# Kernel optimization log

Measured on AMD Instinct MI355X. Metric: run time of the kernel, lower is better.

## Reference

```python
import jax, jax.numpy as jnp
import numpy as np

N_NODES = 50000
N_POOLED = 25000
N_EDGES = 800000
D = 64
NUM_LAYERS = 4
LN_EPS = 1e-5
LEAKY_SLOPE = 0.01


def setup_inputs() -> dict:
    key = jax.random.key(0)
    k_x, k_e, k_i, k_w = jax.random.split(key, 4)
    x = jax.random.normal(k_x, (N_POOLED, D), dtype=jnp.float32)
    edge_index = jax.random.randint(k_e, (2, N_EDGES), 0, N_NODES, dtype=jnp.int64)
    # unique sorted indices of kept nodes (as produced by top-k pooling)
    perm = jax.random.permutation(k_i, N_NODES)
    idx = jnp.sort(perm[:N_POOLED]).astype(jnp.int64)
    Ws = jax.random.normal(k_w, (NUM_LAYERS, D, D), dtype=jnp.float32) / np.sqrt(D)
    bs = jnp.zeros((NUM_LAYERS, D), dtype=jnp.float32)
    gammas = jnp.ones((NUM_LAYERS, D), dtype=jnp.float32)
    betas = jnp.zeros((NUM_LAYERS, D), dtype=jnp.float32)
    return {"x": x, "edge_index": edge_index, "idx": idx,
            "Ws": Ws, "bs": bs, "gammas": gammas, "betas": betas}


def _layer_norm(x, gamma, beta):
    mu = jnp.mean(x, axis=-1, keepdims=True)
    xc = x - mu
    var = jnp.mean(xc * xc, axis=-1, keepdims=True)
    return xc * jax.lax.rsqrt(var + LN_EPS) * gamma + beta


def reference(x, edge_index, idx, Ws, bs, gammas, betas):
    # Unpool (layer 0): scatter pooled features into full-size zero tensor.
    cur = jnp.zeros((N_NODES, D), dtype=x.dtype).at[idx].set(x)

    # GCN normalization with self loops (shared across layers; graph is fixed).
    loop = jnp.arange(N_NODES, dtype=edge_index.dtype)
    src = jnp.concatenate([edge_index[0], loop])
    dst = jnp.concatenate([edge_index[1], loop])
    deg = jax.ops.segment_sum(jnp.ones_like(dst, dtype=x.dtype), dst,
                              num_segments=N_NODES)
    dinv = jax.lax.rsqrt(jnp.maximum(deg, 1.0))  # deg >= 1 (self loops)
    norm = (dinv[src] * dinv[dst])[:, None]      # [E+N, 1]

    h = None
    for l in range(NUM_LAYERS):
        # GCNConv: X W, then D^{-1/2}(A+I)D^{-1/2} aggregation, then bias.
        xw = cur @ Ws[l]
        agg = jax.ops.segment_sum(xw[src] * norm, dst, num_segments=N_NODES)
        agg = agg + bs[l]
        y = _layer_norm(agg, gammas[l], betas[l])
        act = jnp.where(y > 0, y, LEAKY_SLOPE * y)  # LeakyReLU(0.01)
        # dropout p=0.3 is identity in eval mode
        h = act * 0.5 if h is None else h + act * 0.5
        cur = act  # subsequent unpools are identity (sizes already match)
    return h
```

## Files before the change

kernel.cpp:

```cpp
#include <hip/hip_runtime.h>
#include <hip/hip_fp16.h>

#define NN 50000
#define NP 25000
#define NE 800000
#define DD 64
#define NL 4


__device__ __forceinline__ ushort f2bf(float f) {
    unsigned u = __float_as_uint(f);
    unsigned r = (u + 0x7fffu + ((u >> 16) & 1u)) >> 16;
    return (ushort)r;
}

__device__ __forceinline__ float4 bf4_to_f4(uint a, uint b) {
    float4 r;
    r.x = __uint_as_float(a << 16);
    r.y = __uint_as_float(a & 0xffff0000u);
    r.z = __uint_as_float(b << 16);
    r.w = __uint_as_float(b & 0xffff0000u);
    return r;
}

__device__ __forceinline__ float4 ld_bf16x4(const uint2* p) {
    uint2 q = *p;
    return bf4_to_f4(q.x, q.y);
}


__global__ void count_edges_k(const int* __restrict__ dst, int* __restrict__ cnt,
                              int* __restrict__ rank, int E) {
    int e = blockIdx.x * 256 + threadIdx.x;
    if (e < E) rank[e] = atomicAdd(&cnt[dst[e]], 1);
}

__global__ void scan_local_k(const int* __restrict__ cnt, int* __restrict__ rowptr,
                             int* __restrict__ bsum, int n) {
    __shared__ int tmp[1024];
    int t = threadIdx.x;
    int i = blockIdx.x * 1024 + t;
    int v = (i < n) ? cnt[i] : 0;
    tmp[t] = v;
    __syncthreads();
    for (int off = 1; off < 1024; off <<= 1) {
        int a = (t >= off) ? tmp[t - off] : 0;
        __syncthreads();
        tmp[t] += a;
        __syncthreads();
    }
    if (i < n) rowptr[i] = tmp[t] - v;
    if (t == 1023) bsum[blockIdx.x] = tmp[1023];
}

__global__ void finalize_k(int* __restrict__ rowptr, const int* __restrict__ bsum,
                           const int* __restrict__ cnt, float* __restrict__ dinv,
                           int n, int nb) {
    __shared__ int base_sh, total_sh;
    int t = threadIdx.x;
    if (t < 64) {
        int v = (t < nb) ? bsum[t] : 0;
        int s = v;
#pragma unroll
        for (int o = 1; o < 64; o <<= 1) {
            int u = __shfl_up(s, o);
            if (t >= o) s += u;
        }
        if (t == (int)blockIdx.x) base_sh = s - v;
        if (t == nb - 1) total_sh = s;
    }
    __syncthreads();
    int i = blockIdx.x * 1024 + t;
    if (i < n) {
        rowptr[i] += base_sh;
        dinv[i] = rsqrtf((float)(cnt[i] + 1));
    }
    if (i == n) rowptr[n] = total_sh;
}

__global__ void fill_scatter_k(const int* __restrict__ src, const int* __restrict__ dst,
                               const int* __restrict__ rank, const int* __restrict__ rowptr,
                               const float* __restrict__ dinv, uint* __restrict__ csr,
                               const float4* __restrict__ x4, const int* __restrict__ idx,
                               ushort4* __restrict__ c0) {
    int b = blockIdx.x;
    if (b < 3125) {
        int e = b * 256 + threadIdx.x;
        int s = src[e], d = dst[e];
        int p = rowptr[d] + rank[e];
        float w = dinv[s] * dinv[d];
        uint h = (uint)__half_as_ushort(__float2half_rn(w));
        csr[p] = (uint)s | (h << 16);
    } else {
        int i = (b - 3125) * 256 + threadIdx.x;
        if (i >= NP * 16) return;
        int row = i >> 4, q = i & 15;
        float4 v = x4[i];
        ushort4 o;
        o.x = f2bf(v.x); o.y = f2bf(v.y); o.z = f2bf(v.z); o.w = f2bf(v.w);
        c0[(size_t)idx[row] * 16 + q] = o;
    }
}


__global__ void gemm64_k(const uint2* __restrict__ in2, const float* __restrict__ W,
                         ushort* __restrict__ out) {
    __shared__ float sW[64][64];
    __shared__ float srow[16][64];
    int t = threadIdx.x;
    const float4* W4 = (const float4*)W;
    float4* sW4 = (float4*)sW;
#pragma unroll
    for (int j = 0; j < 4; ++j) sW4[t + 256 * j] = W4[t + 256 * j];
    int r0 = blockIdx.x * 16;
    float4 val = ld_bf16x4(in2 + (size_t)r0 * 16 + t);
    *(float4*)&srow[t >> 4][4 * (t & 15)] = val;
    __syncthreads();
    int r = t >> 4;
    int c4 = (t & 15) * 4;
    float ax = 0.f, ay = 0.f, az = 0.f, aw = 0.f;
#pragma unroll
    for (int k = 0; k < 64; ++k) {
        float a = srow[r][k];
        float4 w = *(const float4*)&sW[k][c4];
        ax += a * w.x; ay += a * w.y; az += a * w.z; aw += a * w.w;
    }
    ushort4 o;
    o.x = f2bf(ax); o.y = f2bf(ay); o.z = f2bf(az); o.w = f2bf(aw);
    *(ushort4*)&out[(size_t)(r0 + r) * 64 + c4] = o;
}


__global__ void agg_ln_k(const uint4* __restrict__ xw4, const int* __restrict__ rowptr,
                         const uint* __restrict__ csr, const float* __restrict__ dinv,
                         const float4* __restrict__ bias4, const float4* __restrict__ gamma4,
                         const float4* __restrict__ beta4, uint4* next,
                         const uint4* c1, const uint4* c2, const uint4* c3,
                         float4* outp, int last) {
    int tid = threadIdx.x;
    int l8 = tid & 7;
    int v = blockIdx.x * 32 + (tid >> 3);
    if (v >= NN) return;
    float dv = dinv[v];
    int jb = rowptr[v], je = rowptr[v + 1];
    float4 aLo, aHi;
    {
        uint4 q = xw4[(size_t)v * 8 + l8];
        float4 lo = bf4_to_f4(q.x, q.y), hi = bf4_to_f4(q.z, q.w);
        float s = dv * dv;
        aLo.x = s * lo.x; aLo.y = s * lo.y; aLo.z = s * lo.z; aLo.w = s * lo.w;
        aHi.x = s * hi.x; aHi.y = s * hi.y; aHi.z = s * hi.z; aHi.w = s * hi.w;
    }
#define WGT(E)  __half2float(__ushort_as_half((ushort)((E) >> 16)))
    for (int j = jb; j < je; j += 8) {
        uint e0 = csr[j];
        uint e1 = csr[min(j + 1, je - 1)];
        uint e2 = csr[min(j + 2, je - 1)];
        uint e3 = csr[min(j + 3, je - 1)];
        uint e4 = csr[min(j + 4, je - 1)];
        uint e5 = csr[min(j + 5, je - 1)];
        uint e6 = csr[min(j + 6, je - 1)];
        uint e7 = csr[min(j + 7, je - 1)];
        float w0 = WGT(e0);
        float w1 = (j + 1 < je) ? WGT(e1) : 0.f;
        float w2 = (j + 2 < je) ? WGT(e2) : 0.f;
        float w3 = (j + 3 < je) ? WGT(e3) : 0.f;
        float w4 = (j + 4 < je) ? WGT(e4) : 0.f;
        float w5 = (j + 5 < je) ? WGT(e5) : 0.f;
        float w6 = (j + 6 < je) ? WGT(e6) : 0.f;
        float w7 = (j + 7 < je) ? WGT(e7) : 0.f;
        uint4 q0 = xw4[(size_t)(e0 & 0xffffu) * 8 + l8];
        uint4 q1 = xw4[(size_t)(e1 & 0xffffu) * 8 + l8];
        uint4 q2 = xw4[(size_t)(e2 & 0xffffu) * 8 + l8];
        uint4 q3 = xw4[(size_t)(e3 & 0xffffu) * 8 + l8];
        uint4 q4 = xw4[(size_t)(e4 & 0xffffu) * 8 + l8];
        uint4 q5 = xw4[(size_t)(e5 & 0xffffu) * 8 + l8];
        uint4 q6 = xw4[(size_t)(e6 & 0xffffu) * 8 + l8];
        uint4 q7 = xw4[(size_t)(e7 & 0xffffu) * 8 + l8];
#define ACC(Q, W) { \
        float4 lo = bf4_to_f4(Q.x, Q.y), hi = bf4_to_f4(Q.z, Q.w); \
        aLo.x += W * lo.x; aLo.y += W * lo.y; aLo.z += W * lo.z; aLo.w += W * lo.w; \
        aHi.x += W * hi.x; aHi.y += W * hi.y; aHi.z += W * hi.z; aHi.w += W * hi.w; }
        ACC(q0, w0) ACC(q1, w1) ACC(q2, w2) ACC(q3, w3)
        ACC(q4, w4) ACC(q5, w5) ACC(q6, w6) ACC(q7, w7)
#undef ACC
    }
#undef WGT
    float4 bLo = bias4[2 * l8], bBhi = bias4[2 * l8 + 1];
    aLo.x += bLo.x; aLo.y += bLo.y; aLo.z += bLo.z; aLo.w += bLo.w;
    aHi.x += bBhi.x; aHi.y += bBhi.y; aHi.z += bBhi.z; aHi.w += bBhi.w;
    float s = aLo.x + aLo.y + aLo.z + aLo.w + aHi.x + aHi.y + aHi.z + aHi.w;
#pragma unroll
    for (int o = 1; o <= 4; o <<= 1) s += __shfl_xor(s, o);
    float mu = s * (1.0f / 64.0f);
    float4 cLo = make_float4(aLo.x - mu, aLo.y - mu, aLo.z - mu, aLo.w - mu);
    float4 cHi = make_float4(aHi.x - mu, aHi.y - mu, aHi.z - mu, aHi.w - mu);
    float q2v = cLo.x * cLo.x + cLo.y * cLo.y + cLo.z * cLo.z + cLo.w * cLo.w
              + cHi.x * cHi.x + cHi.y * cHi.y + cHi.z * cHi.z + cHi.w * cHi.w;
#pragma unroll
    for (int o = 1; o <= 4; o <<= 1) q2v += __shfl_xor(q2v, o);
    float rs = rsqrtf(q2v * (1.0f / 64.0f) + 1e-5f);
    float4 gLo = gamma4[2 * l8], gHi = gamma4[2 * l8 + 1];
    float4 tLo = beta4[2 * l8],  tHi = beta4[2 * l8 + 1];
    float4 yLo = make_float4(cLo.x * rs * gLo.x + tLo.x, cLo.y * rs * gLo.y + tLo.y,
                             cLo.z * rs * gLo.z + tLo.z, cLo.w * rs * gLo.w + tLo.w);
    float4 yHi = make_float4(cHi.x * rs * gHi.x + tHi.x, cHi.y * rs * gHi.y + tHi.y,
                             cHi.z * rs * gHi.z + tHi.z, cHi.w * rs * gHi.w + tHi.w);
    float4 eLo = make_float4(yLo.x > 0.f ? yLo.x : 0.01f * yLo.x,
                             yLo.y > 0.f ? yLo.y : 0.01f * yLo.y,
                             yLo.z > 0.f ? yLo.z : 0.01f * yLo.z,
                             yLo.w > 0.f ? yLo.w : 0.01f * yLo.w);
    float4 eHi = make_float4(yHi.x > 0.f ? yHi.x : 0.01f * yHi.x,
                             yHi.y > 0.f ? yHi.y : 0.01f * yHi.y,
                             yHi.z > 0.f ? yHi.z : 0.01f * yHi.z,
                             yHi.w > 0.f ? yHi.w : 0.01f * yHi.w);
    if (!last) {
        uint4 o;
        o.x = (uint)f2bf(eLo.x) | ((uint)f2bf(eLo.y) << 16);
        o.y = (uint)f2bf(eLo.z) | ((uint)f2bf(eLo.w) << 16);
        o.z = (uint)f2bf(eHi.x) | ((uint)f2bf(eHi.y) << 16);
        o.w = (uint)f2bf(eHi.z) | ((uint)f2bf(eHi.w) << 16);
        next[(size_t)v * 8 + l8] = o;
    } else {
        uint4 u1 = c1[(size_t)v * 8 + l8];
        uint4 u2 = c2[(size_t)v * 8 + l8];
        uint4 u3 = c3[(size_t)v * 8 + l8];
        float4 p1 = bf4_to_f4(u1.x, u1.y), p1h = bf4_to_f4(u1.z, u1.w);
        float4 p2 = bf4_to_f4(u2.x, u2.y), p2h = bf4_to_f4(u2.z, u2.w);
        float4 p3 = bf4_to_f4(u3.x, u3.y), p3h = bf4_to_f4(u3.z, u3.w);
        float4 oLo, oHi;
        oLo.x = 0.5f * (p1.x + p2.x + p3.x + eLo.x);
        oLo.y = 0.5f * (p1.y + p2.y + p3.y + eLo.y);
        oLo.z = 0.5f * (p1.z + p2.z + p3.z + eLo.z);
        oLo.w = 0.5f * (p1.w + p2.w + p3.w + eLo.w);
        oHi.x = 0.5f * (p1h.x + p2h.x + p3h.x + eHi.x);
        oHi.y = 0.5f * (p1h.y + p2h.y + p3h.y + eHi.y);
        oHi.z = 0.5f * (p1h.z + p2h.z + p3h.z + eHi.z);
        oHi.w = 0.5f * (p1h.w + p2h.w + p3h.w + eHi.w);
        outp[(size_t)v * 16 + 2 * l8]     = oLo;
        outp[(size_t)v * 16 + 2 * l8 + 1] = oHi;
    }
}


extern "C" void kernel_launch(void* const* d_in, const int* in_sizes, int n_in,
                              void* d_out, int out_size, void* d_ws, size_t ws_size,
                              hipStream_t stream) {
    const float* x      = (const float*)d_in[0];
    const int*   ei     = (const int*)d_in[1];
    const int*   src    = ei;
    const int*   dst    = ei + NE;
    const int*   idx    = (const int*)d_in[2];
    const float* Ws     = (const float*)d_in[3];
    const float* bs     = (const float*)d_in[4];
    const float* gammas = (const float*)d_in[5];
    const float* betas  = (const float*)d_in[6];
    float* out = (float*)d_out;

    char* w = (char*)d_ws;
    auto alloc = [&](size_t bytes) -> char* {
        char* p = w;
        w += (bytes + 255) & ~(size_t)255;
        return p;
    };
    char*   zbase  = w;
    int*    cnt    = (int*)alloc((size_t)NN * 4);
    ushort* c0     = (ushort*)alloc((size_t)NN * 64 * 2);
    size_t  zbytes = (size_t)(w - zbase);
    ushort* c[NL];
    c[0] = c0;
    for (int l = 1; l < NL; ++l) c[l] = (ushort*)alloc((size_t)NN * 64 * 2);
    ushort* xw     = (ushort*)alloc((size_t)NN * 64 * 2);
    int*    rowptr = (int*)alloc((size_t)(NN + 1) * 4);
    int*    rank   = (int*)alloc((size_t)NE * 4);
    float*  dinv   = (float*)alloc((size_t)NN * 4);
    int*    bsum   = (int*)alloc(64 * 4);
    uint*   csr    = (uint*)alloc((size_t)NE * 4);

    hipMemsetAsync(zbase, 0, zbytes, stream);

    count_edges_k<<<(NE + 255) / 256, 256, 0, stream>>>(dst, cnt, rank, NE);
    int nb = (NN + 1023) / 1024;
    scan_local_k<<<nb, 1024, 0, stream>>>(cnt, rowptr, bsum, NN);
    finalize_k<<<nb, 1024, 0, stream>>>(rowptr, bsum, cnt, dinv, NN, nb);
    fill_scatter_k<<<3125 + 1563, 256, 0, stream>>>(src, dst, rank, rowptr, dinv, csr,
                                                    (const float4*)x, idx, (ushort4*)c[0]);

    int agrid = (NN + 31) / 32;
    for (int l = 0; l < NL; ++l) {
        gemm64_k<<<NN / 16, 256, 0, stream>>>((const uint2*)c[l], Ws + (size_t)l * 64 * 64,
                                              xw);
        int last = (l == NL - 1);
        agg_ln_k<<<agrid, 256, 0, stream>>>((const uint4*)xw, rowptr, csr, dinv,
                                            (const float4*)(bs + l * 64),
                                            (const float4*)(gammas + l * 64),
                                            (const float4*)(betas + l * 64),
                                            last ? nullptr : (uint4*)c[l + 1],
                                            (const uint4*)c[1], (const uint4*)c[2],
                                            (const uint4*)c[3], (float4*)out, last);
    }
}
```

Before: 200.0 us.

## Fuse GEMM into aggregation kernel by aggregating before multiplying by W

```diff
diff --git a/kernel.cpp b/kernel.cpp
--- a/kernel.cpp
+++ b/kernel.cpp
@@ -21,11 +21,6 @@
     r.z = __uint_as_float(b << 16);
     r.w = __uint_as_float(b & 0xffff0000u);
     return r;
-}
-
-__device__ __forceinline__ float4 ld_bf16x4(const uint2* p) {
-    uint2 q = *p;
-    return bf4_to_f4(q.x, q.y);
 }
 
 
@@ -103,98 +98,98 @@
 }
 
 
-__global__ void gemm64_k(const uint2* __restrict__ in2, const float* __restrict__ W,
-                         ushort* __restrict__ out) {
+__global__ void agg_mm_ln_k(const uint4* __restrict__ cur4, const int* __restrict__ rowptr,
+                            const uint* __restrict__ csr, const float* __restrict__ dinv,
+                            const float* __restrict__ W,
+                            const float4* __restrict__ bias4,
+                            const float4* __restrict__ gamma4,
+                            const float4* __restrict__ beta4, uint4* next,
+                            const uint4* c1, const uint4* c2, const uint4* c3,
+                            float4* outp, int last) {
     __shared__ float sW[64][64];
-    __shared__ float srow[16][64];
+    __shared__ float sz[32][68];
     int t = threadIdx.x;
-    const float4* W4 = (const float4*)W;
-    float4* sW4 = (float4*)sW;
-#pragma unroll
-    for (int j = 0; j < 4; ++j) sW4[t + 256 * j] = W4[t + 256 * j];
-    int r0 = blockIdx.x * 16;
-    float4 val = ld_bf16x4(in2 + (size_t)r0 * 16 + t);
-    *(float4*)&srow[t >> 4][4 * (t & 15)] = val;
+    {
+        const float4* W4 = (const float4*)W;
+        float4* sW4 = (float4*)sW;
+#pragma unroll
+        for (int j = 0; j < 4; ++j) sW4[t + 256 * j] = W4[t + 256 * j];
+    }
+    int l8 = t & 7;
+    int oct = t >> 3;
+    int v = blockIdx.x * 32 + oct;
+    float4 aLo = make_float4(0.f, 0.f, 0.f, 0.f);
+    float4 aHi = make_float4(0.f, 0.f, 0.f, 0.f);
+    if (v < NN) {
+        float dv = dinv[v];
+        int jb = rowptr[v], je = rowptr[v + 1];
+        {
+            uint4 q = cur4[(size_t)v * 8 + l8];
+            float4 lo = bf4_to_f4(q.x, q.y), hi = bf4_to_f4(q.z, q.w);
+            float s = dv * dv;
+            aLo.x = s * lo.x; aLo.y = s * lo.y; aLo.z = s * lo.z; aLo.w = s * lo.w;
+            aHi.x = s * hi.x; aHi.y = s * hi.y; aHi.z = s * hi.z; aHi.w = s * hi.w;
+        }
+#define WGT(E)  __half2float(__ushort_as_half((ushort)((E) >> 16)))
+        for (int j = jb; j < je; j += 8) {
+            uint e0 = csr[j];
+            uint e1 = csr[min(j + 1, je - 1)];
+            uint e2 = csr[min(j + 2, je - 1)];
+            uint e3 = csr[min(j + 3, je - 1)];
+            uint e4 = csr[min(j + 4, je - 1)];
+            uint e5 = csr[min(j + 5, je - 1)];
+            uint e6 = csr[min(j + 6, je - 1)];
+            uint e7 = csr[min(j + 7, je - 1)];
+            float w0 = WGT(e0);
+            float w1 = (j + 1 < je) ? WGT(e1) : 0.f;
+            float w2 = (j + 2 < je) ? WGT(e2) : 0.f;
+            float w3 = (j + 3 < je) ? WGT(e3) : 0.f;
+            float w4 = (j + 4 < je) ? WGT(e4) : 0.f;
+            float w5 = (j + 5 < je) ? WGT(e5) : 0.f;
+            float w6 = (j + 6 < je) ? WGT(e6) : 0.f;
+            float w7 = (j + 7 < je) ? WGT(e7) : 0.f;
+            uint4 q0 = cur4[(size_t)(e0 & 0xffffu) * 8 + l8];
+            uint4 q1 = cur4[(size_t)(e1 & 0xffffu) * 8 + l8];
+            uint4 q2 = cur4[(size_t)(e2 & 0xffffu) * 8 + l8];
+            uint4 q3 = cur4[(size_t)(e3 & 0xffffu) * 8 + l8];
+            uint4 q4 = cur4[(size_t)(e4 & 0xffffu) * 8 + l8];
+            uint4 q5 = cur4[(size_t)(e5 & 0xffffu) * 8 + l8];
+            uint4 q6 = cur4[(size_t)(e6 & 0xffffu) * 8 + l8];
+            uint4 q7 = cur4[(size_t)(e7 & 0xffffu) * 8 + l8];
+#define ACC(Q, Wt) { \
+            float4 lo = bf4_to_f4(Q.x, Q.y), hi = bf4_to_f4(Q.z, Q.w); \
+            aLo.x += Wt * lo.x; aLo.y += Wt * lo.y; aLo.z += Wt * lo.z; aLo.w += Wt * lo.w; \
+            aHi.x += Wt * hi.x; aHi.y += Wt * hi.y; aHi.z += Wt * hi.z; aHi.w += Wt * hi.w; }
+            ACC(q0, w0) ACC(q1, w1) ACC(q2, w2) ACC(q3, w3)
+            ACC(q4, w4) ACC(q5, w5) ACC(q6, w6) ACC(q7, w7)
+#undef ACC
+        }
+#undef WGT
+    }
+    *(float4*)&sz[oct][8 * l8]     = aLo;
+    *(float4*)&sz[oct][8 * l8 + 4] = aHi;
     __syncthreads();
-    int r = t >> 4;
-    int c4 = (t & 15) * 4;
-    float ax = 0.f, ay = 0.f, az = 0.f, aw = 0.f;
+    int c8 = 8 * l8;
+    float4 y1 = make_float4(0.f, 0.f, 0.f, 0.f);
+    float4 y2 = make_float4(0.f, 0.f, 0.f, 0.f);
 #pragma unroll
     for (int k = 0; k < 64; ++k) {
-        float a = srow[r][k];
-        float4 w = *(const float4*)&sW[k][c4];
-        ax += a * w.x; ay += a * w.y; az += a * w.z; aw += a * w.w;
-    }
-    ushort4 o;
-    o.x = f2bf(ax); o.y = f2bf(ay); o.z = f2bf(az); o.w = f2bf(aw);
-    *(ushort4*)&out[(size_t)(r0 + r) * 64 + c4] = o;
-}
-
-
-__global__ void agg_ln_k(const uint4* __restrict__ xw4, const int* __restrict__ rowptr,
-                         const uint* __restrict__ csr, const float* __restrict__ dinv,
-                         const float4* __restrict__ bias4, const float4* __restrict__ gamma4,
-                         const float4* __restrict__ beta4, uint4* next,
-                         const uint4* c1, const uint4* c2, const uint4* c3,
-                         float4* outp, int last) {
-    int tid = threadIdx.x;
-    int l8 = tid & 7;
-    int v = blockIdx.x * 32 + (tid >> 3);
+        float a = sz[oct][k];
+        float4 w1 = *(const float4*)&sW[k][c8];
+        float4 w2 = *(const float4*)&sW[k][c8 + 4];
+        y1.x += a * w1.x; y1.y += a * w1.y; y1.z += a * w1.z; y1.w += a * w1.w;
+        y2.x += a * w2.x; y2.y += a * w2.y; y2.z += a * w2.z; y2.w += a * w2.w;
+    }
     if (v >= NN) return;
-    float dv = dinv[v];
-    int jb = rowptr[v], je = rowptr[v + 1];
-    float4 aLo, aHi;
-    {
-        uint4 q = xw4[(size_t)v * 8 + l8];
-        float4 lo = bf4_to_f4(q.x, q.y), hi = bf4_to_f4(q.z, q.w);
-        float s = dv * dv;
-        aLo.x = s * lo.x; aLo.y = s * lo.y; aLo.z = s * lo.z; aLo.w = s * lo.w;
-        aHi.x = s * hi.x; aHi.y = s * hi.y; aHi.z = s * hi.z; aHi.w = s * hi.w;
-    }
-#define WGT(E)  __half2float(__ushort_as_half((ushort)((E) >> 16)))
-    for (int j = jb; j < je; j += 8) {
-        uint e0 = csr[j];
-        uint e1 = csr[min(j + 1, je - 1)];
-        uint e2 = csr[min(j + 2, je - 1)];
-        uint e3 = csr[min(j + 3, je - 1)];
-        uint e4 = csr[min(j + 4, je - 1)];
-        uint e5 = csr[min(j + 5, je - 1)];
-        uint e6 = csr[min(j + 6, je - 1)];
-        uint e7 = csr[min(j + 7, je - 1)];
-        float w0 = WGT(e0);
-        float w1 = (j + 1 < je) ? WGT(e1) : 0.f;
-        float w2 = (j + 2 < je) ? WGT(e2) : 0.f;
-        float w3 = (j + 3 < je) ? WGT(e3) : 0.f;
-        float w4 = (j + 4 < je) ? WGT(e4) : 0.f;
-        float w5 = (j + 5 < je) ? WGT(e5) : 0.f;
-        float w6 = (j + 6 < je) ? WGT(e6) : 0.f;
-        float w7 = (j + 7 < je) ? WGT(e7) : 0.f;
-        uint4 q0 = xw4[(size_t)(e0 & 0xffffu) * 8 + l8];
-        uint4 q1 = xw4[(size_t)(e1 & 0xffffu) * 8 + l8];
-        uint4 q2 = xw4[(size_t)(e2 & 0xffffu) * 8 + l8];
-        uint4 q3 = xw4[(size_t)(e3 & 0xffffu) * 8 + l8];
-        uint4 q4 = xw4[(size_t)(e4 & 0xffffu) * 8 + l8];
-        uint4 q5 = xw4[(size_t)(e5 & 0xffffu) * 8 + l8];
-        uint4 q6 = xw4[(size_t)(e6 & 0xffffu) * 8 + l8];
-        uint4 q7 = xw4[(size_t)(e7 & 0xffffu) * 8 + l8];
-#define ACC(Q, W) { \
-        float4 lo = bf4_to_f4(Q.x, Q.y), hi = bf4_to_f4(Q.z, Q.w); \
-        aLo.x += W * lo.x; aLo.y += W * lo.y; aLo.z += W * lo.z; aLo.w += W * lo.w; \
-        aHi.x += W * hi.x; aHi.y += W * hi.y; aHi.z += W * hi.z; aHi.w += W * hi.w; }
-        ACC(q0, w0) ACC(q1, w1) ACC(q2, w2) ACC(q3, w3)
-        ACC(q4, w4) ACC(q5, w5) ACC(q6, w6) ACC(q7, w7)
-#undef ACC
-    }
-#undef WGT
-    float4 bLo = bias4[2 * l8], bBhi = bias4[2 * l8 + 1];
-    aLo.x += bLo.x; aLo.y += bLo.y; aLo.z += bLo.z; aLo.w += bLo.w;
-    aHi.x += bBhi.x; aHi.y += bBhi.y; aHi.z += bBhi.z; aHi.w += bBhi.w;
-    float s = aLo.x + aLo.y + aLo.z + aLo.w + aHi.x + aHi.y + aHi.z + aHi.w;
+    float4 bLo = bias4[2 * l8], bHi = bias4[2 * l8 + 1];
+    y1.x += bLo.x; y1.y += bLo.y; y1.z += bLo.z; y1.w += bLo.w;
+    y2.x += bHi.x; y2.y += bHi.y; y2.z += bHi.z; y2.w += bHi.w;
+    float s = y1.x + y1.y + y1.z + y1.w + y2.x + y2.y + y2.z + y2.w;
 #pragma unroll
     for (int o = 1; o <= 4; o <<= 1) s += __shfl_xor(s, o);
     float mu = s * (1.0f / 64.0f);
-    float4 cLo = make_float4(aLo.x - mu, aLo.y - mu, aLo.z - mu, aLo.w - mu);
-    float4 cHi = make_float4(aHi.x - mu, aHi.y - mu, aHi.z - mu, aHi.w - mu);
+    float4 cLo = make_float4(y1.x - mu, y1.y - mu, y1.z - mu, y1.w - mu);
+    float4 cHi = make_float4(y2.x - mu, y2.y - mu, y2.z - mu, y2.w - mu);
     float q2v = cLo.x * cLo.x + cLo.y * cLo.y + cLo.z * cLo.z + cLo.w * cLo.w
               + cHi.x * cHi.x + cHi.y * cHi.y + cHi.z * cHi.z + cHi.w * cHi.w;
 #pragma unroll
@@ -267,10 +262,9 @@
     int*    cnt    = (int*)alloc((size_t)NN * 4);
     ushort* c0     = (ushort*)alloc((size_t)NN * 64 * 2);
     size_t  zbytes = (size_t)(w - zbase);
-    ushort* c[NL];
+    ushort* c[NL + 1];
     c[0] = c0;
-    for (int l = 1; l < NL; ++l) c[l] = (ushort*)alloc((size_t)NN * 64 * 2);
-    ushort* xw     = (ushort*)alloc((size_t)NN * 64 * 2);
+    for (int l = 1; l <= NL; ++l) c[l] = (ushort*)alloc((size_t)NN * 64 * 2);
     int*    rowptr = (int*)alloc((size_t)(NN + 1) * 4);
     int*    rank   = (int*)alloc((size_t)NE * 4);
     float*  dinv   = (float*)alloc((size_t)NN * 4);
@@ -288,15 +282,14 @@
 
     int agrid = (NN + 31) / 32;
     for (int l = 0; l < NL; ++l) {
-        gemm64_k<<<NN / 16, 256, 0, stream>>>((const uint2*)c[l], Ws + (size_t)l * 64 * 64,
-                                              xw);
         int last = (l == NL - 1);
-        agg_ln_k<<<agrid, 256, 0, stream>>>((const uint4*)xw, rowptr, csr, dinv,
-                                            (const float4*)(bs + l * 64),
-                                            (const float4*)(gammas + l * 64),
-                                            (const float4*)(betas + l * 64),
-                                            last ? nullptr : (uint4*)c[l + 1],
-                                            (const uint4*)c[1], (const uint4*)c[2],
-                                            (const uint4*)c[3], (float4*)out, last);
-    }
-}
+        agg_mm_ln_k<<<agrid, 256, 0, stream>>>((const uint4*)c[l], rowptr, csr, dinv,
+                                               Ws + (size_t)l * 64 * 64,
+                                               (const float4*)(bs + l * 64),
+                                               (const float4*)(gammas + l * 64),
+                                               (const float4*)(betas + l * 64),
+                                               last ? nullptr : (uint4*)c[l + 1],
+                                               (const uint4*)c[1], (const uint4*)c[2],
+                                               (const uint4*)c[3], (float4*)out, last);
+    }
+}
```

Measured after the change: 170.0 us. -15.0%, faster.
